# Kernel optimization log

Hardware: AMD Instinct MI355X
Metric: run time of the kernel (lower is better)

## Reference

```python
import jax, jax.numpy as jnp
import numpy as np

D_MODEL = 1024
N_HEADS = 16
HEAD_DIM = D_MODEL // N_HEADS


def setup_inputs() -> dict:
    key = jax.random.key(0)
    k1, k2, k3 = jax.random.split(key, 3)
    x = jax.random.normal(k1, (2, 2048, D_MODEL), dtype=jnp.float32)
    # nn.Linear weights: stored as [out, in]; y = x @ W.T
    W_qkv = jax.random.normal(k2, (3 * D_MODEL, D_MODEL), dtype=jnp.float32) * (1.0 / np.sqrt(D_MODEL))
    W_out = jax.random.normal(k3, (D_MODEL, D_MODEL), dtype=jnp.float32) * (1.0 / np.sqrt(D_MODEL))
    return {"x": x, "W_qkv": W_qkv, "W_out": W_out}


def reference(x, W_qkv, W_out):
    B, T, C = x.shape
    qkv = jnp.einsum('btc,oc->bto', x, W_qkv)  # [B,T,3C]
    q, k, v = jnp.split(qkv, 3, axis=-1)

    def split_heads(t):
        return t.reshape(B, T, N_HEADS, HEAD_DIM).transpose(0, 2, 1, 3)  # [B,H,T,D]

    q, k, v = split_heads(q), split_heads(k), split_heads(v)
    scale = jnp.asarray(1.0 / np.sqrt(HEAD_DIM), dtype=x.dtype)
    attn = jnp.einsum('bhqd,bhkd->bhqk', q, k) * scale  # [B,H,T,T]
    causal = jnp.tril(jnp.ones((T, T), dtype=bool))
    attn = jnp.where(causal, attn, -jnp.inf)
    attn = jax.nn.softmax(attn, axis=-1)
    out = jnp.einsum('bhqk,bhkd->bhqd', attn, v)
    out = out.transpose(0, 2, 1, 3).reshape(B, T, C)
    return jnp.einsum('btc,oc->bto', out, W_out)
```

## Files before the change

kernel.cpp:

```cpp
#include <hip/hip_runtime.h>

typedef float f32x4 __attribute__((ext_vector_type(4)));
typedef short short8 __attribute__((ext_vector_type(8)));

#define GBL(p) ((__attribute__((address_space(1))) void*)(p))
#define LDS(p) ((__attribute__((address_space(3))) void*)(p))

static __device__ __forceinline__ unsigned short f2bf(float x) {
  union { float f; unsigned u; } a; a.f = x;
  unsigned u = a.u;
  return (unsigned short)((u + 0x7FFFu + ((u >> 16) & 1u)) >> 16);
}

static __device__ __forceinline__ short8 ld8(const unsigned short* p) {
  return *(const short8*)(p);
}

static __device__ __forceinline__ f32x4 zero4() {
  f32x4 z = {0.f, 0.f, 0.f, 0.f};
  return z;
}

__global__ void cvt_kernel(const float4* __restrict__ in, ushort4* __restrict__ out, int n4) {
  int i = blockIdx.x * blockDim.x + threadIdx.x;
  if (i >= n4) return;
  float4 v = in[i];
  ushort4 o;
  o.x = f2bf(v.x); o.y = f2bf(v.y); o.z = f2bf(v.z); o.w = f2bf(v.w);
  out[i] = o;
}

template<int MODE>
__global__ __launch_bounds__(256) void gemm_bt(
    const unsigned short* __restrict__ A,
    const unsigned short* __restrict__ B,
    void* __restrict__ Cout, void* __restrict__ Cout2, void* __restrict__ Cout3,
    int M, int N, int K)
{
  __shared__ __align__(16) unsigned short As[128 * 32];
  __shared__ __align__(16) unsigned short Bs[128 * 32];

  const int t = threadIdx.x;
  const int lane = t & 63;
  const int w = t >> 6;
  const int wr = (w >> 1) * 64;
  const int wc = (w & 1) * 64;
  const int fr = lane & 15;
  const int kg = lane >> 4;
  const size_t rowBase = (size_t)blockIdx.y * 128;
  const size_t colBase = (size_t)blockIdx.x * 128;

  f32x4 acc[4][4];
  for (int m = 0; m < 4; ++m)
    for (int n = 0; n < 4; ++n) acc[m][n] = zero4();

  const unsigned short* ag = A + (rowBase + (t >> 2)) * (size_t)K + (t & 3) * 8;
  const unsigned short* bg = B + (colBase + (t >> 2)) * (size_t)K + (t & 3) * 8;
  unsigned short* asd = As + t * 8;
  unsigned short* bsd = Bs + t * 8;

  for (int k0 = 0; k0 < K; k0 += 32) {
    __builtin_amdgcn_global_load_lds(GBL(ag + k0),                   LDS(asd),        16, 0, 0);
    __builtin_amdgcn_global_load_lds(GBL(ag + (size_t)64 * K + k0),  LDS(asd + 2048), 16, 0, 0);
    __builtin_amdgcn_global_load_lds(GBL(bg + k0),                   LDS(bsd),        16, 0, 0);
    __builtin_amdgcn_global_load_lds(GBL(bg + (size_t)64 * K + k0),  LDS(bsd + 2048), 16, 0, 0);
    __syncthreads();
    short8 af[4], bf[4];
    for (int m = 0; m < 4; ++m) af[m] = ld8(As + (wr + m * 16 + fr) * 32 + kg * 8);
    for (int n = 0; n < 4; ++n) bf[n] = ld8(Bs + (wc + n * 16 + fr) * 32 + kg * 8);
    for (int m = 0; m < 4; ++m)
      for (int n = 0; n < 4; ++n)
        acc[m][n] = __builtin_amdgcn_mfma_f32_16x16x32_bf16(af[m], bf[n], acc[m][n], 0, 0, 0);
    __syncthreads();
  }

  for (int m = 0; m < 4; ++m)
    for (int n = 0; n < 4; ++n) {
      const size_t row = rowBase + wr + m * 16 + kg * 4;
      const size_t col = colBase + wc + n * 16 + fr;
      if (MODE == 0) {
        float* C = (float*)Cout;
        for (int j = 0; j < 4; ++j) C[(row + j) * N + col] = acc[m][n][j];
      } else {
        if (col < 1024) {
          unsigned short* Q = (unsigned short*)Cout;
          for (int j = 0; j < 4; ++j)
            Q[(row + j) * 1024 + col] = f2bf(acc[m][n][j] * 0.18033688f);
        } else if (col < 2048) {
          unsigned short* KF = (unsigned short*)Cout2;
          const int d_all = (int)col - 1024;
          const int hh = d_all >> 6, d = d_all & 63;
          const int c = d >> 5, kgp = (d >> 3) & 3, el = d & 7;
          for (int j = 0; j < 4; ++j) {
            const int r = (int)row + j;
            const int bp = r >> 11, s = r & 2047;
            const size_t addr =
                ((size_t)(((bp * 16 + hh) * 128 + (s >> 4)) * 2 + c)) * 512
                + (size_t)((kgp * 16 + (s & 15)) * 8 + el);
            KF[addr] = f2bf(acc[m][n][j]);
          }
        } else {
          unsigned short* VF = (unsigned short*)Cout3;
          const int d_all = (int)col - 2048;
          const int hh = d_all >> 6, dd = d_all & 63;
          const int nd = dd >> 4, frp = dd & 15;
          const int r0 = (int)row;
          const int bp = r0 >> 11, s = r0 & 2047;
          const size_t base =
              ((size_t)(((bp * 16 + hh) * 64 + (s >> 5)) * 4 + nd)) * 512
              + (size_t)((((s >> 3) & 3) * 16 + frp) * 8 + (s & 7));
          ushort4 o4;
          o4.x = f2bf(acc[m][n][0]); o4.y = f2bf(acc[m][n][1]);
          o4.z = f2bf(acc[m][n][2]); o4.w = f2bf(acc[m][n][3]);
          *(ushort4*)(VF + base) = o4;
        }
      }
    }
}

__global__ __launch_bounds__(256) void attn_kernel(
    const unsigned short* __restrict__ qb,
    const unsigned short* __restrict__ kfb,
    const unsigned short* __restrict__ vfb,
    unsigned short* __restrict__ om)
{
  __shared__ __align__(16) unsigned short Ps[4][16 * 32];

  const int bh = blockIdx.x;
  const int pr = blockIdx.y;
  const int b = bh >> 4, h = bh & 15;
  const int t = threadIdx.x;
  const int lane = t & 63, w = t >> 6;
  const int fr = lane & 15, kg = lane >> 4;
  const int lane8 = lane * 8;
  const size_t seq0 = (size_t)b * 2048;

  unsigned short* pw = &Ps[w][0];
  const unsigned short* kfB = kfb + (size_t)bh * (128 * 2 * 512) + lane8;
  const unsigned short* vfB = vfb + (size_t)bh * (64 * 4 * 512) + lane8;

  unsigned short* pws0[4];
  unsigned short* pws1[4];
#pragma unroll
  for (int j = 0; j < 4; ++j) {
    const int r = kg * 4 + j;
    pws0[j] = pw + r * 32 + ((((fr >> 3)     ^ kg) & 3) << 3) + (fr & 7);
    pws1[j] = pw + r * 32 + ((((2 + (fr >> 3)) ^ kg) & 3) << 3) + (fr & 7);
  }
  const int rdswz = fr * 32 + (((kg ^ (fr >> 2)) & 3) << 3);

#define LOADK(kr0, kf) do {                                                    \
    const unsigned short* kp = kfB + (size_t)((kr0) >> 4) * 1024;              \
    kf[0] = ld8(kp);        kf[1] = ld8(kp + 512);                             \
    kf[2] = ld8(kp + 1024); kf[3] = ld8(kp + 1536);                            \
  } while (0)

#define LOADV(kr0, vf) do {                                                    \
    const unsigned short* vp = vfB + (size_t)((kr0) >> 5) * 2048;              \
    vf[0] = ld8(vp);        vf[1] = ld8(vp + 512);                             \
    vf[2] = ld8(vp + 1024); vf[3] = ld8(vp + 1536);                            \
  } while (0)

#define QKSM(kr0, kf, DOMASK) do {                                             \
    f32x4 s0 = zero4(), s1 = zero4();                                          \
    __builtin_amdgcn_s_setprio(1);                                             \
    s0 = __builtin_amdgcn_mfma_f32_16x16x32_bf16(qf0, kf[0], s0, 0, 0, 0);     \
    s0 = __builtin_amdgcn_mfma_f32_16x16x32_bf16(qf1, kf[1], s0, 0, 0, 0);     \
    s1 = __builtin_amdgcn_mfma_f32_16x16x32_bf16(qf0, kf[2], s1, 0, 0, 0);     \
    s1 = __builtin_amdgcn_mfma_f32_16x16x32_bf16(qf1, kf[3], s1, 0, 0, 0);     \
    __builtin_amdgcn_s_setprio(0);                                             \
    _Pragma("unroll")                                                          \
    for (int j = 0; j < 4; ++j) {                                              \
      float a0 = s0[j];                                                        \
      float a1 = s1[j];                                                        \
      if (DOMASK) {                                                            \
        const int qrow = qrow0 + kg * 4 + j;                                   \
        a0 = ((kr0) + fr      <= qrow) ? a0 : -1e30f;                          \
        a1 = ((kr0) + 16 + fr <= qrow) ? a1 : -1e30f;                          \
      }                                                                        \
      const float e0 = exp2f(a0);                                              \
      const float e1 = exp2f(a1);                                              \
      l_run[j] += e0 + e1;                                                     \
      *pws0[j] = f2bf(e0);                                                     \
      *pws1[j] = f2bf(e1);                                                     \
    }                                                                          \
  } while (0)

#define PV(vf) do {                                                            \
    __builtin_amdgcn_s_setprio(1);                                             \
    _Pragma("unroll")                                                          \
    for (int nd = 0; nd < 4; ++nd)                                             \
      o[nd] = __builtin_amdgcn_mfma_f32_16x16x32_bf16(pf, vf[nd], o[nd], 0, 0, 0); \
    __builtin_amdgcn_s_setprio(0);                                             \
  } while (0)

#define READP do { pf = ld8(pw + rdswz); } while (0)

  for (int half = 0; half < 2; ++half) {
    const int qt = half ? (31 - pr) : pr;
    const int qrow0 = qt * 64 + w * 16;
    const int nfull = qrow0 >> 5;

    const unsigned short* qp = qb + (seq0 + qrow0 + fr) * 1024 + h * 64;
    const short8 qf0 = ld8(qp + kg * 8);
    const short8 qf1 = ld8(qp + 32 + kg * 8);

    float l_run[4] = {0.f, 0.f, 0.f, 0.f};
    f32x4 o[4];
    for (int n = 0; n < 4; ++n) o[n] = zero4();

    short8 kA[4], kB[4], vA[4], vB[4], pf;
    LOADK(0, kA);
    int kt = 0;
    while (true) {
      {
        const int kn = (kt < nfull) ? (kt + 1) * 32 : nfull * 32;
        LOADK(kn, kB);
        LOADV(kt * 32, vA);
        if (kt == nfull) { QKSM(kt * 32, kA, 1); } else { QKSM(kt * 32, kA, 0); }
        if (kt > 0) PV(vB);
        READP;
      }
      if (kt == nfull) { PV(vA); break; }
      ++kt;
      {
        const int kn = (kt < nfull) ? (kt + 1) * 32 : nfull * 32;
        LOADK(kn, kA);
        LOADV(kt * 32, vB);
        if (kt == nfull) { QKSM(kt * 32, kB, 1); } else { QKSM(kt * 32, kB, 0); }
        PV(vA);
        READP;
      }
      if (kt == nfull) { PV(vB); break; }
      ++kt;
    }

    for (int j = 0; j < 4; ++j) {
      float l = l_run[j];
      l += __shfl_xor(l, 1);
      l += __shfl_xor(l, 2);
      l += __shfl_xor(l, 4);
      l += __shfl_xor(l, 8);
      const float inv = 1.0f / l;
      for (int nd = 0; nd < 4; ++nd) {
        om[(seq0 + qrow0 + kg * 4 + j) * 1024 + h * 64 + nd * 16 + fr] =
            f2bf(o[nd][j] * inv);
      }
    }
  }
#undef LOADK
#undef LOADV
#undef QKSM
#undef PV
#undef READP
}

extern "C" void kernel_launch(void* const* d_in, const int* in_sizes, int n_in,
                              void* d_out, int out_size, void* d_ws, size_t ws_size,
                              hipStream_t stream) {
  const float* x    = (const float*)d_in[0];
  const float* Wqkv = (const float*)d_in[1];
  const float* Wout = (const float*)d_in[2];
  float* out = (float*)d_out;

  char* ws = (char*)d_ws;
  unsigned short* xb    = (unsigned short*)(ws);
  unsigned short* wqkvb = (unsigned short*)(ws + 8388608);
  unsigned short* woutb = (unsigned short*)(ws + 14680064);
  unsigned short* qbuf  = (unsigned short*)(ws + 16777216);
  unsigned short* kfb   = (unsigned short*)(ws + 25165824);
  unsigned short* vfb   = (unsigned short*)(ws + 33554432);
  unsigned short* attno = (unsigned short*)(ws + 41943040);

  cvt_kernel<<<dim3(4096), dim3(256), 0, stream>>>((const float4*)x,    (ushort4*)xb,    1048576);
  cvt_kernel<<<dim3(3072), dim3(256), 0, stream>>>((const float4*)Wqkv, (ushort4*)wqkvb, 786432);
  cvt_kernel<<<dim3(1024), dim3(256), 0, stream>>>((const float4*)Wout, (ushort4*)woutb, 262144);

  gemm_bt<1><<<dim3(24, 32), dim3(256), 0, stream>>>(xb, wqkvb, (void*)qbuf, (void*)kfb, (void*)vfb, 4096, 3072, 1024);

  attn_kernel<<<dim3(32, 16), dim3(256), 0, stream>>>(qbuf, kfb, vfb, attno);

  gemm_bt<0><<<dim3(8, 32), dim3(256), 0, stream>>>(attno, woutb, (void*)out, nullptr, nullptr, 4096, 1024, 1024);
}
```

Before: 193.5 us.

## Fuse conversions, swizzle GEMM block order, split attention tiles, shrink output GEMM tile

Merges the three fp32-to-bf16 conversion launches into one kernel. Both GEMMs get a block-index remap that interleaves tiles across 8 groups, aimed at better L2/XCD locality. The attention kernel no longer pairs a short and a long causal query tile per block; each block handles one tile (grid doubled, heavy tiles launched first) with launch_bounds set for 4 blocks per CU. The output projection uses 64x128 tiles so it launches twice as many blocks and fills the GPU better, at the cost of less reuse per block.

```diff
diff --git a/kernel.cpp b/kernel.cpp
--- a/kernel.cpp
+++ b/kernel.cpp
@@ -21,17 +21,21 @@
   return z;
 }
 
-__global__ void cvt_kernel(const float4* __restrict__ in, ushort4* __restrict__ out, int n4) {
+__global__ void cvt3_kernel(const float4* __restrict__ x,    ushort4* __restrict__ xo,
+                            const float4* __restrict__ wq,   ushort4* __restrict__ wqo,
+                            const float4* __restrict__ wo,   ushort4* __restrict__ woo) {
   int i = blockIdx.x * blockDim.x + threadIdx.x;
-  if (i >= n4) return;
-  float4 v = in[i];
+  const float4* in; ushort4* out; int j;
+  if (i < 1048576)      { in = x;  out = xo;  j = i; }
+  else if (i < 1835008) { in = wq; out = wqo; j = i - 1048576; }
+  else                  { in = wo; out = woo; j = i - 1835008; }
+  float4 v = in[j];
   ushort4 o;
   o.x = f2bf(v.x); o.y = f2bf(v.y); o.z = f2bf(v.z); o.w = f2bf(v.w);
-  out[i] = o;
-}
-
-template<int MODE>
-__global__ __launch_bounds__(256) void gemm_bt(
+  out[j] = o;
+}
+
+__global__ __launch_bounds__(256) void gemm_qkv(
     const unsigned short* __restrict__ A,
     const unsigned short* __restrict__ B,
     void* __restrict__ Cout, void* __restrict__ Cout2, void* __restrict__ Cout3,
@@ -47,8 +51,13 @@
   const int wc = (w & 1) * 64;
   const int fr = lane & 15;
   const int kg = lane >> 4;
-  const size_t rowBase = (size_t)blockIdx.y * 128;
-  const size_t colBase = (size_t)blockIdx.x * 128;
+
+  const int lin = blockIdx.y * gridDim.x + blockIdx.x;
+  const int cpx = (gridDim.x * gridDim.y) >> 3;
+  const int l2 = (lin & 7) * cpx + (lin >> 3);
+  const int bx = l2 % gridDim.x, by = l2 / gridDim.x;
+  const size_t rowBase = (size_t)by * 128;
+  const size_t colBase = (size_t)bx * 128;
 
   f32x4 acc[4][4];
   for (int m = 0; m < 4; ++m)
@@ -78,47 +87,96 @@
     for (int n = 0; n < 4; ++n) {
       const size_t row = rowBase + wr + m * 16 + kg * 4;
       const size_t col = colBase + wc + n * 16 + fr;
-      if (MODE == 0) {
-        float* C = (float*)Cout;
-        for (int j = 0; j < 4; ++j) C[(row + j) * N + col] = acc[m][n][j];
+      if (col < 1024) {
+        unsigned short* Q = (unsigned short*)Cout;
+        for (int j = 0; j < 4; ++j)
+          Q[(row + j) * 1024 + col] = f2bf(acc[m][n][j] * 0.18033688f);
+      } else if (col < 2048) {
+        unsigned short* KF = (unsigned short*)Cout2;
+        const int d_all = (int)col - 1024;
+        const int hh = d_all >> 6, d = d_all & 63;
+        const int c = d >> 5, kgp = (d >> 3) & 3, el = d & 7;
+        for (int j = 0; j < 4; ++j) {
+          const int r = (int)row + j;
+          const int bp = r >> 11, s = r & 2047;
+          const size_t addr =
+              ((size_t)(((bp * 16 + hh) * 128 + (s >> 4)) * 2 + c)) * 512
+              + (size_t)((kgp * 16 + (s & 15)) * 8 + el);
+          KF[addr] = f2bf(acc[m][n][j]);
+        }
       } else {
-        if (col < 1024) {
-          unsigned short* Q = (unsigned short*)Cout;
-          for (int j = 0; j < 4; ++j)
-            Q[(row + j) * 1024 + col] = f2bf(acc[m][n][j] * 0.18033688f);
-        } else if (col < 2048) {
-          unsigned short* KF = (unsigned short*)Cout2;
-          const int d_all = (int)col - 1024;
-          const int hh = d_all >> 6, d = d_all & 63;
-          const int c = d >> 5, kgp = (d >> 3) & 3, el = d & 7;
-          for (int j = 0; j < 4; ++j) {
-            const int r = (int)row + j;
-            const int bp = r >> 11, s = r & 2047;
-            const size_t addr =
-                ((size_t)(((bp * 16 + hh) * 128 + (s >> 4)) * 2 + c)) * 512
-                + (size_t)((kgp * 16 + (s & 15)) * 8 + el);
-            KF[addr] = f2bf(acc[m][n][j]);
-          }
-        } else {
-          unsigned short* VF = (unsigned short*)Cout3;
-          const int d_all = (int)col - 2048;
-          const int hh = d_all >> 6, dd = d_all & 63;
-          const int nd = dd >> 4, frp = dd & 15;
-          const int r0 = (int)row;
-          const int bp = r0 >> 11, s = r0 & 2047;
-          const size_t base =
-              ((size_t)(((bp * 16 + hh) * 64 + (s >> 5)) * 4 + nd)) * 512
-              + (size_t)((((s >> 3) & 3) * 16 + frp) * 8 + (s & 7));
-          ushort4 o4;
-          o4.x = f2bf(acc[m][n][0]); o4.y = f2bf(acc[m][n][1]);
-          o4.z = f2bf(acc[m][n][2]); o4.w = f2bf(acc[m][n][3]);
-          *(ushort4*)(VF + base) = o4;
-        }
+        unsigned short* VF = (unsigned short*)Cout3;
+        const int d_all = (int)col - 2048;
+        const int hh = d_all >> 6, dd = d_all & 63;
+        const int nd = dd >> 4, frp = dd & 15;
+        const int r0 = (int)row;
+        const int bp = r0 >> 11, s = r0 & 2047;
+        const size_t base =
+            ((size_t)(((bp * 16 + hh) * 64 + (s >> 5)) * 4 + nd)) * 512
+            + (size_t)((((s >> 3) & 3) * 16 + frp) * 8 + (s & 7));
+        ushort4 o4;
+        o4.x = f2bf(acc[m][n][0]); o4.y = f2bf(acc[m][n][1]);
+        o4.z = f2bf(acc[m][n][2]); o4.w = f2bf(acc[m][n][3]);
+        *(ushort4*)(VF + base) = o4;
       }
     }
 }
 
-__global__ __launch_bounds__(256) void attn_kernel(
+__global__ __launch_bounds__(256) void gemm_out(
+    const unsigned short* __restrict__ A,
+    const unsigned short* __restrict__ B,
+    float* __restrict__ C, int M, int N, int K)
+{
+  __shared__ __align__(16) unsigned short As[64 * 32];
+  __shared__ __align__(16) unsigned short Bs[128 * 32];
+
+  const int t = threadIdx.x;
+  const int lane = t & 63;
+  const int w = t >> 6;
+  const int wr = (w >> 1) * 32;
+  const int wc = (w & 1) * 64;
+  const int fr = lane & 15;
+  const int kg = lane >> 4;
+
+  const int lin = blockIdx.y * gridDim.x + blockIdx.x;
+  const int cpx = (gridDim.x * gridDim.y) >> 3;
+  const int l2 = (lin & 7) * cpx + (lin >> 3);
+  const int bx = l2 % gridDim.x, by = l2 / gridDim.x;
+  const size_t rowBase = (size_t)by * 64;
+  const size_t colBase = (size_t)bx * 128;
+
+  f32x4 acc[2][4];
+  for (int m = 0; m < 2; ++m)
+    for (int n = 0; n < 4; ++n) acc[m][n] = zero4();
+
+  const unsigned short* ag = A + (rowBase + (t >> 2)) * (size_t)K + (t & 3) * 8;
+  const unsigned short* bg = B + (colBase + (t >> 2)) * (size_t)K + (t & 3) * 8;
+  unsigned short* asd = As + t * 8;
+  unsigned short* bsd = Bs + t * 8;
+
+  for (int k0 = 0; k0 < K; k0 += 32) {
+    __builtin_amdgcn_global_load_lds(GBL(ag + k0),                   LDS(asd),        16, 0, 0);
+    __builtin_amdgcn_global_load_lds(GBL(bg + k0),                   LDS(bsd),        16, 0, 0);
+    __builtin_amdgcn_global_load_lds(GBL(bg + (size_t)64 * K + k0),  LDS(bsd + 2048), 16, 0, 0);
+    __syncthreads();
+    short8 af[2], bf[4];
+    for (int m = 0; m < 2; ++m) af[m] = ld8(As + (wr + m * 16 + fr) * 32 + kg * 8);
+    for (int n = 0; n < 4; ++n) bf[n] = ld8(Bs + (wc + n * 16 + fr) * 32 + kg * 8);
+    for (int m = 0; m < 2; ++m)
+      for (int n = 0; n < 4; ++n)
+        acc[m][n] = __builtin_amdgcn_mfma_f32_16x16x32_bf16(af[m], bf[n], acc[m][n], 0, 0, 0);
+    __syncthreads();
+  }
+
+  for (int m = 0; m < 2; ++m)
+    for (int n = 0; n < 4; ++n) {
+      const size_t row = rowBase + wr + m * 16 + kg * 4;
+      const size_t col = colBase + wc + n * 16 + fr;
+      for (int j = 0; j < 4; ++j) C[(row + j) * N + col] = acc[m][n][j];
+    }
+}
+
+__global__ __launch_bounds__(256, 4) void attn_kernel(
     const unsigned short* __restrict__ qb,
     const unsigned short* __restrict__ kfb,
     const unsigned short* __restrict__ vfb,
@@ -127,7 +185,7 @@
   __shared__ __align__(16) unsigned short Ps[4][16 * 32];
 
   const int bh = blockIdx.x;
-  const int pr = blockIdx.y;
+  const int qt = 31 - blockIdx.y;
   const int b = bh >> 4, h = bh & 15;
   const int t = threadIdx.x;
   const int lane = t & 63, w = t >> 6;
@@ -144,7 +202,7 @@
 #pragma unroll
   for (int j = 0; j < 4; ++j) {
     const int r = kg * 4 + j;
-    pws0[j] = pw + r * 32 + ((((fr >> 3)     ^ kg) & 3) << 3) + (fr & 7);
+    pws0[j] = pw + r * 32 + ((((fr >> 3)       ^ kg) & 3) << 3) + (fr & 7);
     pws1[j] = pw + r * 32 + ((((2 + (fr >> 3)) ^ kg) & 3) << 3) + (fr & 7);
   }
   const int rdswz = fr * 32 + (((kg ^ (fr >> 2)) & 3) << 3);
@@ -196,8 +254,7 @@
 
 #define READP do { pf = ld8(pw + rdswz); } while (0)
 
-  for (int half = 0; half < 2; ++half) {
-    const int qt = half ? (31 - pr) : pr;
+  {
     const int qrow0 = qt * 64 + w * 16;
     const int nfull = qrow0 >> 5;
 
@@ -272,13 +329,15 @@
   unsigned short* vfb   = (unsigned short*)(ws + 33554432);
   unsigned short* attno = (unsigned short*)(ws + 41943040);
 
-  cvt_kernel<<<dim3(4096), dim3(256), 0, stream>>>((const float4*)x,    (ushort4*)xb,    1048576);
-  cvt_kernel<<<dim3(3072), dim3(256), 0, stream>>>((const float4*)Wqkv, (ushort4*)wqkvb, 786432);
-  cvt_kernel<<<dim3(1024), dim3(256), 0, stream>>>((const float4*)Wout, (ushort4*)woutb, 262144);
-
-  gemm_bt<1><<<dim3(24, 32), dim3(256), 0, stream>>>(xb, wqkvb, (void*)qbuf, (void*)kfb, (void*)vfb, 4096, 3072, 1024);
-
-  attn_kernel<<<dim3(32, 16), dim3(256), 0, stream>>>(qbuf, kfb, vfb, attno);
-
-  gemm_bt<0><<<dim3(8, 32), dim3(256), 0, stream>>>(attno, woutb, (void*)out, nullptr, nullptr, 4096, 1024, 1024);
-}
+  cvt3_kernel<<<dim3(8192), dim3(256), 0, stream>>>(
+      (const float4*)x,    (ushort4*)xb,
+      (const float4*)Wqkv, (ushort4*)wqkvb,
+      (const float4*)Wout, (ushort4*)woutb);
+
+  gemm_qkv<<<dim3(24, 32), dim3(256), 0, stream>>>(
+      xb, wqkvb, (void*)qbuf, (void*)kfb, (void*)vfb, 4096, 3072, 1024);
+
+  attn_kernel<<<dim3(32, 32), dim3(256), 0, stream>>>(qbuf, kfb, vfb, attno);
+
+  gemm_out<<<dim3(8, 64), dim3(256), 0, stream>>>(attno, woutb, out, 4096, 1024, 1024);
+}
```

Result: slower. 223.2 us (+15.4%).
